# Kernel tuning notes

Measured on AMD Instinct MI355X. Metric: run time of the kernel, lower is better.

Reference implementation:

```python
import jax, jax.numpy as jnp
import numpy as np

N, E = 25000, 400000
NF, EF, HNF, HEF = 32, 32, 128, 128
NOUT, EOUT = 32, 32
D_N, D_E = HNF + NF, HEF + EF  # concat dims fed to the GNN layer


def _glorot(key, shape):
    return jax.random.normal(key, shape, jnp.float32) / np.sqrt(shape[0])


def setup_inputs() -> dict:
    key = jax.random.key(0)
    ks = jax.random.split(key, 10)
    return {
        "nf": jax.random.normal(ks[0], (N, NF), jnp.float32),
        "ef": jax.random.normal(ks[1], (E, EF), jnp.float32),
        "src": jax.random.randint(ks[2], (E,), 0, N),
        "dst": jax.random.randint(ks[3], (E,), 0, N),
        # AttnMPNNLayer params: edge model, attention logit model, node model
        "W_edge": _glorot(ks[4], (2 * D_N + D_E, HEF)),
        "b_edge": jnp.zeros((HEF,), jnp.float32),
        "W_attn": _glorot(ks[5], (2 * D_N + D_E, 1)),
        "b_attn": jnp.zeros((1,), jnp.float32),
        "W_node": _glorot(ks[6], (D_N + HEF, HNF)),
        "b_node": jnp.zeros((HNF,), jnp.float32),
        # output heads (MLP with num_neurons=[] -> single Linear)
        "W_nout": _glorot(ks[7], (HNF, NOUT)),
        "b_nout": jnp.zeros((NOUT,), jnp.float32),
        "W_eout": _glorot(ks[8], (HEF, EOUT)),
        "b_eout": jnp.zeros((EOUT,), jnp.float32),
        "n_iters": 3,
    }


def _attn_mpnn_layer(hnf, hef, src, dst, W_edge, b_edge, W_attn, b_attn, W_node, b_node):
    """Attention message passing: gather endpoints, edge MLP + attn logit,
    edge-softmax over incoming edges (per dst node), scatter-aggregate, node MLP."""
    n = hnf.shape[0]
    e_in = jnp.concatenate([hnf[src], hnf[dst], hef], axis=-1)   # [E, 2*D_N + D_E]
    m = jax.nn.relu(e_in @ W_edge + b_edge)                      # [E, HEF] new edge feats
    logit = (e_in @ W_attn + b_attn)[:, 0]                       # [E]
    # numerically stable edge softmax grouped by destination node
    lmax = jax.ops.segment_max(logit, dst, num_segments=n)
    lmax = jnp.where(jnp.isfinite(lmax), lmax, 0.0)              # isolated nodes -> 0
    a = jnp.exp(logit - lmax[dst])
    denom = jax.ops.segment_sum(a, dst, num_segments=n)
    alpha = a / jnp.maximum(denom[dst], 1e-16)
    agg = jax.ops.segment_sum(alpha[:, None] * m, dst, num_segments=n)  # [N, HEF]
    un = jax.nn.relu(jnp.concatenate([hnf, agg], axis=-1) @ W_node + b_node)  # [N, HNF]
    return un, m


def reference(nf, ef, src, dst, W_edge, b_edge, W_attn, b_attn, W_node, b_node,
              W_nout, b_nout, W_eout, b_eout, n_iters):
    hnf = jnp.zeros((nf.shape[0], HNF), nf.dtype)
    hef = jnp.zeros((ef.shape[0], HEF), ef.dtype)
    for _ in range(n_iters):
        hnf = jnp.concatenate([hnf, nf], axis=-1)   # input re-injection
        hef = jnp.concatenate([hef, ef], axis=-1)
        hnf, hef = _attn_mpnn_layer(hnf, hef, src, dst,
                                    W_edge, b_edge, W_attn, b_attn, W_node, b_node)
    unf = hnf @ W_nout + b_nout
    uef = hef @ W_eout + b_eout
    return unf, uef
```

## Files before the change

### kernel.cpp

```cpp
#include <hip/hip_runtime.h>


#define GN 25000
#define GE 400000
#define NODE_BLKS 196
#define EDGE_BLKS 3125

typedef unsigned short u16;
typedef __attribute__((ext_vector_type(8))) short bf16x8;
typedef __attribute__((ext_vector_type(4))) float f32x4;

__device__ inline float b2f(u16 v) {
  union { unsigned int u; float f; } x; x.u = ((unsigned int)v) << 16; return x.f;
}
__device__ inline u16 f2b(float f) {
  union { float f; unsigned int u; } x; x.f = f;
  unsigned int u = x.u;
  u += 0x7fffu + ((u >> 16) & 1u);
  return (u16)(u >> 16);
}

__global__ void detect_dtype(const void* nf, int* flag) {
  if (blockIdx.x == 0 && threadIdx.x == 0) {
    const u16* p = (const u16*)nf;
    int cnt = 0;
    for (int i = 0; i < 512; i += 2) {
      int e = (p[i] >> 7) & 0xFF;
      if (e >= 0x70 && e <= 0x85) cnt++;
    }
    *flag = (cnt < 128) ? 1 : 0;
  }
}

__global__ void convert_kernel(const void* src, u16* dst, long n, const int* flag) {
  int f32 = *flag;
  long i = (long)blockIdx.x * blockDim.x + threadIdx.x;
  long stride = (long)gridDim.x * blockDim.x;
  for (; i < n; i += stride)
    dst[i] = f32 ? f2b(((const float*)src)[i]) : ((const u16*)src)[i];
}

__global__ void gather_ef(const void* ef, const int* eid, u16* efc, const int* flag) {
  int f32 = *flag;
  long idx = (long)blockIdx.x * blockDim.x + threadIdx.x;
  long stride = (long)gridDim.x * blockDim.x;
  long ntot = (long)GE * 32;
  for (; idx < ntot; idx += stride) {
    long j = idx >> 5;
    int c = (int)(idx & 31);
    long e = eid[j];
    efc[idx] = f32 ? f2b(((const float*)ef)[e * 32 + c]) : ((const u16*)ef)[e * 32 + c];
  }
}

__global__ void gather_meta(const int* src, const int* dst, const int* eid,
                            int* srcs, int* dsts, int n) {
  int j = blockIdx.x * blockDim.x + threadIdx.x;
  if (j < n) { int e = eid[j]; srcs[j] = src[e]; dsts[j] = dst[e]; }
}

__global__ void prep_weights(const u16* We, const u16* Wn, const u16* Won, const u16* Woe,
                             u16* WeT, u16* WnpT, u16* WnuT, u16* WoN, u16* WoE) {
  int tid = blockIdx.x * blockDim.x + threadIdx.x;
  int nt = gridDim.x * blockDim.x;
  for (int i = tid; i < 128 * 160; i += nt) { int n = i / 160, k = i % 160; WeT[i] = We[(320 + k) * 128 + n]; }
  for (int i = tid; i < 256 * 160; i += nt) {
    int c = i / 160, k = i % 160;
    WnpT[i] = (c < 128) ? We[k * 128 + c] : We[(160 + k) * 128 + (c - 128)];
  }
  for (int i = tid; i < 128 * 288; i += nt) { int c = i / 288, k = i % 288; WnuT[i] = Wn[k * 128 + c]; }
  for (int i = tid; i < 32 * 128; i += nt) {
    int c = i / 128, k = i % 128;
    WoN[i] = Won[k * 32 + c];
    WoE[i] = Woe[k * 32 + c];
  }
}

__global__ void hist_kernel(const int* dst, int* counts, int n) {
  for (int e = blockIdx.x * blockDim.x + threadIdx.x; e < n; e += gridDim.x * blockDim.x)
    atomicAdd(&counts[dst[e]], 1);
}

__global__ __launch_bounds__(256) void scan_kernel(int* cursor, int* rowptr, int n) {
  __shared__ int part[256];
  int t = threadIdx.x;
  int per = (n + 255) / 256;
  int lo = t * per;
  int hi = lo + per; if (hi > n) hi = n;
  if (lo > n) lo = n;
  int s = 0;
  for (int i = lo; i < hi; ++i) s += cursor[i];
  part[t] = s;
  __syncthreads();
  for (int off = 1; off < 256; off <<= 1) {
    int v = (t >= off) ? part[t - off] : 0;
    __syncthreads();
    part[t] += v;
    __syncthreads();
  }
  int run = (t > 0) ? part[t - 1] : 0;
  for (int i = lo; i < hi; ++i) {
    int c = cursor[i];
    cursor[i] = run;
    rowptr[i + 1] = run + c;
    run += c;
  }
  if (t == 0) rowptr[0] = 0;
}

__global__ void fill_kernel(const int* dst, int* cursor, int* eid, int n) {
  for (int e = blockIdx.x * blockDim.x + threadIdx.x; e < n; e += gridDim.x * blockDim.x) {
    int p = atomicAdd(&cursor[dst[e]], 1);
    eid[p] = e;
  }
}

__global__ __launch_bounds__(256)
void node_proj(const u16* HNF, const u16* nf, const u16* WnpT, const u16* W_attn,
               u16* Xs, u16* Xd, float* as_, float* ad_, int kc0, int nrows) {
  __shared__ union {
    struct { __align__(16) u16 A[128][40]; __align__(16) u16 B[128][40]; } st;
    u16 C[128][130];
  } sm;
  __shared__ float dotbuf[128][2];
  int sel = blockIdx.y, blk = blockIdx.x, tid = threadIdx.x;
  int lane = tid & 63, wv = tid >> 6, wr = wv & 1, wc = wv >> 1;
  const u16* BT = WnpT + sel * 128 * 160;
  u16* OUT = sel ? Xd : Xs;
  float* AOUT = sel ? ad_ : as_;
  const u16* wa = W_attn + sel * 160;
  f32x4 acc[4][4];
  f32x4 zf = {0.f, 0.f, 0.f, 0.f};
  for (int i = 0; i < 4; ++i) for (int j = 0; j < 4; ++j) acc[i][j] = zf;
  float dp = 0.f;
  int arow = tid >> 1, ahalf = (tid & 1) * 16;
  int r0 = blk * 128;
  for (int kc = kc0; kc < 5; ++kc) {
    {
      int r = r0 + arow;
      uint4 v0 = make_uint4(0, 0, 0, 0), v1 = make_uint4(0, 0, 0, 0);
      if (r < nrows) {
        const uint4* p = (kc < 4) ? (const uint4*)(HNF + (size_t)r * 128 + kc * 32 + ahalf)
                                  : (const uint4*)(nf + (size_t)r * 32 + ahalf);
        v0 = p[0]; v1 = p[1];
      }
      *(uint4*)&sm.st.A[arow][ahalf] = v0;
      *(uint4*)&sm.st.A[arow][ahalf + 8] = v1;
    }
    {
      const uint4* p = (const uint4*)(BT + arow * 160 + kc * 32 + ahalf);
      uint4 v0 = p[0], v1 = p[1];
      *(uint4*)&sm.st.B[arow][ahalf] = v0;
      *(uint4*)&sm.st.B[arow][ahalf + 8] = v1;
    }
    __syncthreads();
    {
      float s = 0.f;
      for (int j = 0; j < 16; ++j) s += b2f(sm.st.A[arow][ahalf + j]) * b2f(wa[kc * 32 + ahalf + j]);
      dp += s;
    }
    int q = lane >> 4, l16 = lane & 15;
    bf16x8 af[4], bfr[4];
    for (int i = 0; i < 4; ++i) af[i] = *(const bf16x8*)&sm.st.A[wr * 64 + i * 16 + l16][q * 8];
    for (int j = 0; j < 4; ++j) bfr[j] = *(const bf16x8*)&sm.st.B[wc * 64 + j * 16 + l16][q * 8];
    for (int i = 0; i < 4; ++i)
      for (int j = 0; j < 4; ++j)
        acc[i][j] = __builtin_amdgcn_mfma_f32_16x16x32_bf16(af[i], bfr[j], acc[i][j], 0, 0, 0);
    __syncthreads();
  }
  dotbuf[arow][tid & 1] = dp;
  {
    int q = lane >> 4, l16 = lane & 15;
    for (int i = 0; i < 4; ++i)
      for (int j = 0; j < 4; ++j) {
        int col = wc * 64 + j * 16 + l16;
        for (int rr = 0; rr < 4; ++rr) {
          int row = wr * 64 + i * 16 + q * 4 + rr;
          sm.C[row][col] = f2b(acc[i][j][rr]);
        }
      }
  }
  __syncthreads();
  if (tid < 128) {
    int r = r0 + tid;
    if (r < nrows) AOUT[r] = dotbuf[tid][0] + dotbuf[tid][1];
  }
  {
    int r = tid >> 1, h = (tid & 1) * 64;
    int rg = r0 + r;
    if (rg < nrows) {
      uint4* po = (uint4*)(OUT + (size_t)rg * 128 + h);
      for (int k = 0; k < 8; ++k) {
        unsigned int a0 = *(const unsigned int*)&sm.C[r][h + k * 8];
        unsigned int a1 = *(const unsigned int*)&sm.C[r][h + k * 8 + 2];
        unsigned int a2 = *(const unsigned int*)&sm.C[r][h + k * 8 + 4];
        unsigned int a3 = *(const unsigned int*)&sm.C[r][h + k * 8 + 6];
        po[k] = make_uint4(a0, a1, a2, a3);
      }
    }
  }
}

__global__ __launch_bounds__(256, 4)
void edge_fused(u16* HEF, const u16* ef, const u16* WeT, const u16* W_attn,
                const u16* b_edge, const u16* b_attn, const int* srcs, const int* dsts,
                const u16* Xs, const u16* Xd, const float* as_, const float* ad_,
                float* logit, int kc0) {
  __shared__ union {
    struct { __align__(16) u16 A[128][40]; __align__(16) u16 B[128][40]; } st;
    float C[128][65];
  } sm;
  __shared__ float dotbuf[128];
  int blk = blockIdx.x, tid = threadIdx.x;
  int lane = tid & 63, wv = tid >> 6, wr = wv & 1, wc = wv >> 1;
  int q = lane >> 4, l16 = lane & 15;
  f32x4 acc[4][4];
  f32x4 zf = {0.f, 0.f, 0.f, 0.f};
  for (int i = 0; i < 4; ++i) for (int j = 0; j < 4; ++j) acc[i][j] = zf;
  float dp[4] = {0.f, 0.f, 0.f, 0.f};
  int arow = tid >> 1, ahalf = (tid & 1) * 16;
  long e0 = (long)blk * 128;
  const u16* wa = W_attn + 320;
  for (int kc = kc0; kc < 5; ++kc) {
    {
      long e = e0 + arow;
      const uint4* p = (kc < 4) ? (const uint4*)(HEF + e * 128 + kc * 32 + ahalf)
                                : (const uint4*)(ef + e * 32 + ahalf);
      uint4 v0 = p[0], v1 = p[1];
      *(uint4*)&sm.st.A[arow][ahalf] = v0;
      *(uint4*)&sm.st.A[arow][ahalf + 8] = v1;
    }
    {
      const uint4* p = (const uint4*)(WeT + arow * 160 + kc * 32 + ahalf);
      uint4 v0 = p[0], v1 = p[1];
      *(uint4*)&sm.st.B[arow][ahalf] = v0;
      *(uint4*)&sm.st.B[arow][ahalf + 8] = v1;
    }
    __syncthreads();
    bf16x8 af[4], bfr[4];
    for (int i = 0; i < 4; ++i) af[i] = *(const bf16x8*)&sm.st.A[wr * 64 + i * 16 + l16][q * 8];
    for (int j = 0; j < 4; ++j) bfr[j] = *(const bf16x8*)&sm.st.B[wc * 64 + j * 16 + l16][q * 8];
    if (wc == 0) {
      bf16x8 wv8 = *(const bf16x8*)&wa[kc * 32 + q * 8];
      float wf[8];
      for (int j = 0; j < 8; ++j) wf[j] = b2f((u16)wv8[j]);
      for (int i = 0; i < 4; ++i)
        for (int j = 0; j < 8; ++j) dp[i] += b2f((u16)af[i][j]) * wf[j];
    }
    for (int i = 0; i < 4; ++i)
      for (int j = 0; j < 4; ++j)
        acc[i][j] = __builtin_amdgcn_mfma_f32_16x16x32_bf16(af[i], bfr[j], acc[i][j], 0, 0, 0);
    __syncthreads();
  }
  if (wc == 0) {
    for (int i = 0; i < 4; ++i) {
      dp[i] += __shfl_xor(dp[i], 16);
      dp[i] += __shfl_xor(dp[i], 32);
    }
    if (q == 0)
      for (int i = 0; i < 4; ++i) dotbuf[wr * 64 + i * 16 + l16] = dp[i];
  }
  int r = tid >> 1;
  int h2 = (tid & 1) * 32;
  long e = e0 + r;
  int s = srcs[e], d = dsts[e];
  for (int p = 0; p < 2; ++p) {
    uint4 gvs[4], gvd[4];
    {
      const uint4* ps = (const uint4*)(Xs + (size_t)s * 128 + p * 64 + h2);
      const uint4* pd = (const uint4*)(Xd + (size_t)d * 128 + p * 64 + h2);
      for (int k = 0; k < 4; ++k) { gvs[k] = ps[k]; gvd[k] = pd[k]; }
    }
    if (wc == p) {
      for (int i = 0; i < 4; ++i)
        for (int j = 0; j < 4; ++j) {
          int col = j * 16 + l16;
          float bb = b2f(b_edge[p * 64 + col]);
          for (int rr = 0; rr < 4; ++rr) {
            int row = wr * 64 + i * 16 + q * 4 + rr;
            sm.C[row][col] = acc[i][j][rr] + bb;
          }
        }
    }
    __syncthreads();
    if (p == 0 && tid < 128) {
      long ee = e0 + tid;
      logit[ee] = dotbuf[tid] + as_[srcs[ee]] + ad_[dsts[ee]] + b2f(b_attn[0]);
    }
    uint4 o[4];
    for (int k = 0; k < 4; ++k) {
      unsigned int ov[4];
      for (int w = 0; w < 4; ++w) {
        int c = h2 + k * 8 + 2 * w;
        float c0 = sm.C[r][c], c1 = sm.C[r][c + 1];
        unsigned int us = ((const unsigned int*)&gvs[k])[w];
        unsigned int ud = ((const unsigned int*)&gvd[k])[w];
        float v0 = c0 + b2f((u16)(us & 0xffffu)) + b2f((u16)(ud & 0xffffu));
        float v1 = c1 + b2f((u16)(us >> 16)) + b2f((u16)(ud >> 16));
        v0 = fmaxf(v0, 0.f);
        v1 = fmaxf(v1, 0.f);
        ov[w] = (unsigned int)f2b(v0) | ((unsigned int)f2b(v1) << 16);
      }
      o[k] = make_uint4(ov[0], ov[1], ov[2], ov[3]);
    }
    {
      uint4* po = (uint4*)(HEF + e * 128 + p * 64 + h2);
      for (int k = 0; k < 4; ++k) po[k] = o[k];
    }
    if (p == 0) __syncthreads();
  }
}

__global__ __launch_bounds__(256)
void aggregate(const int* rowptr, const float* logit, const u16* M, u16* AGG, int nrows) {
  int gw = (blockIdx.x * blockDim.x + threadIdx.x) >> 6;
  int lane = threadIdx.x & 63;
  if (gw >= nrows) return;
  int beg = rowptr[gw], end = rowptr[gw + 1];
  float acc0 = 0.f, acc1 = 0.f;
  if (beg < end) {
    float mx = -1e30f;
    for (int j = beg + lane; j < end; j += 64) mx = fmaxf(mx, logit[j]);
    for (int off = 32; off > 0; off >>= 1) mx = fmaxf(mx, __shfl_xor(mx, off));
    float denom = 0.f;
    for (int j = beg; j < end; ++j) {
      float w = __expf(logit[j] - mx);
      denom += w;
      unsigned int mm = *(const unsigned int*)(M + (size_t)j * 128 + 2 * lane);
      acc0 += w * b2f((u16)(mm & 0xffffu));
      acc1 += w * b2f((u16)(mm >> 16));
    }
    float inv = 1.0f / fmaxf(denom, 1e-16f);
    acc0 *= inv; acc1 *= inv;
  }
  unsigned int out = (unsigned int)f2b(acc0) | ((unsigned int)f2b(acc1) << 16);
  *(unsigned int*)(AGG + (size_t)gw * 128 + 2 * lane) = out;
}

__global__ __launch_bounds__(256)
void node_update(u16* HNF, const u16* nf, const u16* AGG, const u16* WnuT,
                 const u16* b_node, int kc0, int nrows) {
  __shared__ union {
    struct { __align__(16) u16 A[128][40]; __align__(16) u16 B[128][40]; } st;
    u16 C[128][130];
  } sm;
  int blk = blockIdx.x, tid = threadIdx.x;
  int lane = tid & 63, wv = tid >> 6, wr = wv & 1, wc = wv >> 1;
  f32x4 acc[4][4];
  f32x4 zf = {0.f, 0.f, 0.f, 0.f};
  for (int i = 0; i < 4; ++i) for (int j = 0; j < 4; ++j) acc[i][j] = zf;
  int arow = tid >> 1, ahalf = (tid & 1) * 16;
  int r0 = blk * 128;
  for (int kc = kc0; kc < 9; ++kc) {
    {
      int r = r0 + arow;
      uint4 v0 = make_uint4(0, 0, 0, 0), v1 = make_uint4(0, 0, 0, 0);
      if (r < nrows) {
        const u16* p;
        if (kc < 4) p = HNF + (size_t)r * 128 + kc * 32 + ahalf;
        else if (kc == 4) p = nf + (size_t)r * 32 + ahalf;
        else p = AGG + (size_t)r * 128 + (kc - 5) * 32 + ahalf;
        v0 = ((const uint4*)p)[0];
        v1 = ((const uint4*)p)[1];
      }
      *(uint4*)&sm.st.A[arow][ahalf] = v0;
      *(uint4*)&sm.st.A[arow][ahalf + 8] = v1;
    }
    {
      const uint4* p = (const uint4*)(WnuT + arow * 288 + kc * 32 + ahalf);
      uint4 v0 = p[0], v1 = p[1];
      *(uint4*)&sm.st.B[arow][ahalf] = v0;
      *(uint4*)&sm.st.B[arow][ahalf + 8] = v1;
    }
    __syncthreads();
    int q = lane >> 4, l16 = lane & 15;
    bf16x8 af[4], bfr[4];
    for (int i = 0; i < 4; ++i) af[i] = *(const bf16x8*)&sm.st.A[wr * 64 + i * 16 + l16][q * 8];
    for (int j = 0; j < 4; ++j) bfr[j] = *(const bf16x8*)&sm.st.B[wc * 64 + j * 16 + l16][q * 8];
    for (int i = 0; i < 4; ++i)
      for (int j = 0; j < 4; ++j)
        acc[i][j] = __builtin_amdgcn_mfma_f32_16x16x32_bf16(af[i], bfr[j], acc[i][j], 0, 0, 0);
    __syncthreads();
  }
  int q = lane >> 4, l16 = lane & 15;
  for (int i = 0; i < 4; ++i)
    for (int j = 0; j < 4; ++j) {
      int col = wc * 64 + j * 16 + l16;
      float bb = b2f(b_node[col]);
      for (int rr = 0; rr < 4; ++rr) {
        int row = wr * 64 + i * 16 + q * 4 + rr;
        sm.C[row][col] = f2b(fmaxf(acc[i][j][rr] + bb, 0.f));
      }
    }
  __syncthreads();
  {
    int r = tid >> 1, h = (tid & 1) * 64;
    int rg = r0 + r;
    if (rg < nrows) {
      uint4* po = (uint4*)(HNF + (size_t)rg * 128 + h);
      for (int k = 0; k < 8; ++k) {
        unsigned int a0 = *(const unsigned int*)&sm.C[r][h + k * 8];
        unsigned int a1 = *(const unsigned int*)&sm.C[r][h + k * 8 + 2];
        unsigned int a2 = *(const unsigned int*)&sm.C[r][h + k * 8 + 4];
        unsigned int a3 = *(const unsigned int*)&sm.C[r][h + k * 8 + 6];
        po[k] = make_uint4(a0, a1, a2, a3);
      }
    }
  }
}

__global__ __launch_bounds__(256)
void head_kernel(const u16* IN, const u16* WT, const u16* bias, float* OUT, long R,
                 const int* remap) {
  __shared__ __align__(16) u16 Asm[128][40];
  __shared__ __align__(16) u16 Bsm[32][40];
  int blk = blockIdx.x, tid = threadIdx.x;
  int lane = tid & 63, wv = tid >> 6;
  f32x4 acc[2][2];
  f32x4 zf = {0.f, 0.f, 0.f, 0.f};
  for (int i = 0; i < 2; ++i) for (int j = 0; j < 2; ++j) acc[i][j] = zf;
  int arow = tid >> 1, ahalf = (tid & 1) * 16;
  long r0 = (long)blk * 128;
  for (int kc = 0; kc < 4; ++kc) {
    {
      long r = r0 + arow;
      uint4 v0 = make_uint4(0, 0, 0, 0), v1 = make_uint4(0, 0, 0, 0);
      if (r < R) {
        const uint4* p = (const uint4*)(IN + r * 128 + kc * 32 + ahalf);
        v0 = p[0]; v1 = p[1];
      }
      *(uint4*)&Asm[arow][ahalf] = v0;
      *(uint4*)&Asm[arow][ahalf + 8] = v1;
    }
    if (tid < 64) {
      const uint4* p = (const uint4*)(WT + arow * 128 + kc * 32 + ahalf);
      uint4 v0 = p[0], v1 = p[1];
      *(uint4*)&Bsm[arow][ahalf] = v0;
      *(uint4*)&Bsm[arow][ahalf + 8] = v1;
    }
    __syncthreads();
    int q = lane >> 4, l16 = lane & 15;
    bf16x8 af[2], bfr[2];
    for (int i = 0; i < 2; ++i) af[i] = *(const bf16x8*)&Asm[wv * 32 + i * 16 + l16][q * 8];
    for (int j = 0; j < 2; ++j) bfr[j] = *(const bf16x8*)&Bsm[j * 16 + l16][q * 8];
    for (int i = 0; i < 2; ++i)
      for (int j = 0; j < 2; ++j)
        acc[i][j] = __builtin_amdgcn_mfma_f32_16x16x32_bf16(af[i], bfr[j], acc[i][j], 0, 0, 0);
    __syncthreads();
  }
  int q = lane >> 4, l16 = lane & 15;
  for (int i = 0; i < 2; ++i)
    for (int rr = 0; rr < 4; ++rr) {
      long r = r0 + wv * 32 + i * 16 + q * 4 + rr;
      if (r < R) {
        long ro = remap ? (long)remap[r] : r;
        for (int j = 0; j < 2; ++j) {
          int col = j * 16 + l16;
          OUT[ro * 32 + col] = acc[i][j][rr] + b2f(bias[col]);
        }
      }
    }
}

extern "C" void kernel_launch(void* const* d_in, const int* in_sizes, int n_in,
                              void* d_out, int out_size, void* d_ws, size_t ws_size,
                              hipStream_t stream) {
  const size_t REQUIRED = 160000000;
  if (ws_size < REQUIRED) return;

  const void* nf_r = d_in[0];
  const void* ef_r = d_in[1];
  const int* src = (const int*)d_in[2];
  const int* dst = (const int*)d_in[3];

  char* ws = (char*)d_ws;
  auto alloc = [&](size_t bytes) {
    char* p = ws;
    ws += (bytes + 255) & ~(size_t)255;
    return p;
  };
  u16* HEF = (u16*)alloc((size_t)GE * 128 * 2);
  u16* HNF = (u16*)alloc((size_t)GN * 128 * 2);
  u16* Xs = (u16*)alloc((size_t)GN * 128 * 2);
  u16* Xd = (u16*)alloc((size_t)GN * 128 * 2);
  float* as_ = (float*)alloc((size_t)GN * 4);
  float* ad_ = (float*)alloc((size_t)GN * 4);
  float* logit = (float*)alloc((size_t)GE * 4);
  int* rowptr = (int*)alloc((size_t)(GN + 1) * 4);
  int* cursor = (int*)alloc((size_t)GN * 4);
  int* eid = (int*)alloc((size_t)GE * 4);
  int* srcs = (int*)alloc((size_t)GE * 4);
  int* dsts = (int*)alloc((size_t)GE * 4);
  u16* WeT = (u16*)alloc(128 * 160 * 2);
  u16* WnpT = (u16*)alloc(256 * 160 * 2);
  u16* WnuT = (u16*)alloc(128 * 288 * 2);
  u16* WoN = (u16*)alloc(32 * 128 * 2);
  u16* WoE = (u16*)alloc(32 * 128 * 2);
  u16* nfc = (u16*)alloc((size_t)GN * 32 * 2);
  u16* efc = (u16*)alloc((size_t)GE * 32 * 2);
  u16* Wec = (u16*)alloc(480 * 128 * 2);
  u16* bec = (u16*)alloc(128 * 2);
  u16* Wac = (u16*)alloc(480 * 2);
  u16* bac = (u16*)alloc(2);
  u16* Wnc = (u16*)alloc(288 * 128 * 2);
  u16* bnc = (u16*)alloc(128 * 2);
  u16* Wnoc = (u16*)alloc(128 * 32 * 2);
  u16* bnoc = (u16*)alloc(32 * 2);
  u16* Weoc = (u16*)alloc(128 * 32 * 2);
  u16* beoc = (u16*)alloc(32 * 2);
  int* dflag = (int*)alloc(4);
  u16* AGG = Xs;

  detect_dtype<<<1, 64, 0, stream>>>(nf_r, dflag);
  hipMemsetAsync(cursor, 0, (size_t)GN * 4, stream);
  hist_kernel<<<1563, 256, 0, stream>>>(dst, cursor, GE);
  scan_kernel<<<1, 256, 0, stream>>>(cursor, rowptr, GN);
  fill_kernel<<<1563, 256, 0, stream>>>(dst, cursor, eid, GE);

  convert_kernel<<<784, 256, 0, stream>>>(nf_r, nfc, (long)GN * 32, dflag);
  gather_ef<<<6250, 256, 0, stream>>>(ef_r, eid, efc, dflag);
  gather_meta<<<1563, 256, 0, stream>>>(src, dst, eid, srcs, dsts, GE);
  convert_kernel<<<240, 256, 0, stream>>>(d_in[4], Wec, 480 * 128, dflag);
  convert_kernel<<<1, 128, 0, stream>>>(d_in[5], bec, 128, dflag);
  convert_kernel<<<2, 256, 0, stream>>>(d_in[6], Wac, 480, dflag);
  convert_kernel<<<1, 64, 0, stream>>>(d_in[7], bac, 1, dflag);
  convert_kernel<<<144, 256, 0, stream>>>(d_in[8], Wnc, 288 * 128, dflag);
  convert_kernel<<<1, 128, 0, stream>>>(d_in[9], bnc, 128, dflag);
  convert_kernel<<<16, 256, 0, stream>>>(d_in[10], Wnoc, 128 * 32, dflag);
  convert_kernel<<<1, 64, 0, stream>>>(d_in[11], bnoc, 32, dflag);
  convert_kernel<<<16, 256, 0, stream>>>(d_in[12], Weoc, 128 * 32, dflag);
  convert_kernel<<<1, 64, 0, stream>>>(d_in[13], beoc, 32, dflag);
  prep_weights<<<128, 256, 0, stream>>>(Wec, Wnc, Wnoc, Weoc, WeT, WnpT, WnuT, WoN, WoE);

  for (int iter = 0; iter < 3; ++iter) {
    int kc0 = (iter == 0) ? 4 : 0;
    dim3 npgrid(NODE_BLKS, 2);
    node_proj<<<npgrid, 256, 0, stream>>>(HNF, nfc, WnpT, Wac, Xs, Xd, as_, ad_, kc0, GN);
    edge_fused<<<EDGE_BLKS, 256, 0, stream>>>(HEF, efc, WeT, Wac, bec, bac, srcs, dsts,
                                              Xs, Xd, as_, ad_, logit, kc0);
    aggregate<<<(GN + 3) / 4, 256, 0, stream>>>(rowptr, logit, HEF, AGG, GN);
    node_update<<<NODE_BLKS, 256, 0, stream>>>(HNF, nfc, AGG, WnuT, bnc, kc0, GN);
  }

  float* out_nf = (float*)d_out;
  float* out_ef = (float*)d_out + (size_t)GN * 32;
  head_kernel<<<NODE_BLKS, 256, 0, stream>>>(HNF, WoN, bnoc, out_nf, GN, nullptr);
  head_kernel<<<EDGE_BLKS, 256, 0, stream>>>(HEF, WoE, beoc, out_ef, GE, eid);
}
```

Before: 700.9 us.

## Shrink edge tiles, prefetch operands, vectorize aggregate, fuse setup kernels

```diff
diff --git a/kernel.cpp b/kernel.cpp
--- a/kernel.cpp
+++ b/kernel.cpp
@@ -4,7 +4,8 @@
 #define GN 25000
 #define GE 400000
 #define NODE_BLKS 196
-#define EDGE_BLKS 3125
+#define EDGE_BLKS 6250
+#define HEAD_EBLKS 3125
 
 typedef unsigned short u16;
 typedef __attribute__((ext_vector_type(8))) short bf16x8;
@@ -53,27 +54,34 @@
   }
 }
 
-__global__ void gather_meta(const int* src, const int* dst, const int* eid,
-                            int* srcs, int* dsts, int n) {
-  int j = blockIdx.x * blockDim.x + threadIdx.x;
-  if (j < n) { int e = eid[j]; srcs[j] = src[e]; dsts[j] = dst[e]; }
-}
-
-__global__ void prep_weights(const u16* We, const u16* Wn, const u16* Won, const u16* Woe,
-                             u16* WeT, u16* WnpT, u16* WnuT, u16* WoN, u16* WoE) {
+__global__ void prep_weights(const void* We, const void* Wn, const void* Wa,
+                             const void* Won, const void* Woe,
+                             const void* be, const void* ba, const void* bn,
+                             const void* bno, const void* beo,
+                             u16* WeT, u16* WnpT, u16* WnuT, u16* WoN, u16* WoE,
+                             u16* Wac, u16* bec, u16* bac, u16* bnc, u16* bnoc, u16* beoc,
+                             const int* flag) {
+  int f32 = *flag;
+  auto ld = [&](const void* p, long i) -> u16 {
+    return f32 ? f2b(((const float*)p)[i]) : ((const u16*)p)[i];
+  };
   int tid = blockIdx.x * blockDim.x + threadIdx.x;
   int nt = gridDim.x * blockDim.x;
-  for (int i = tid; i < 128 * 160; i += nt) { int n = i / 160, k = i % 160; WeT[i] = We[(320 + k) * 128 + n]; }
+  for (int i = tid; i < 128 * 160; i += nt) { int n = i / 160, k = i % 160; WeT[i] = ld(We, (long)(320 + k) * 128 + n); }
   for (int i = tid; i < 256 * 160; i += nt) {
     int c = i / 160, k = i % 160;
-    WnpT[i] = (c < 128) ? We[k * 128 + c] : We[(160 + k) * 128 + (c - 128)];
-  }
-  for (int i = tid; i < 128 * 288; i += nt) { int c = i / 288, k = i % 288; WnuT[i] = Wn[k * 128 + c]; }
+    WnpT[i] = (c < 128) ? ld(We, (long)k * 128 + c) : ld(We, (long)(160 + k) * 128 + (c - 128));
+  }
+  for (int i = tid; i < 128 * 288; i += nt) { int c = i / 288, k = i % 288; WnuT[i] = ld(Wn, (long)k * 128 + c); }
   for (int i = tid; i < 32 * 128; i += nt) {
     int c = i / 128, k = i % 128;
-    WoN[i] = Won[k * 32 + c];
-    WoE[i] = Woe[k * 32 + c];
-  }
+    WoN[i] = ld(Won, (long)k * 32 + c);
+    WoE[i] = ld(Woe, (long)k * 32 + c);
+  }
+  for (int i = tid; i < 480; i += nt) Wac[i] = ld(Wa, i);
+  for (int i = tid; i < 128; i += nt) { bec[i] = ld(be, i); bnc[i] = ld(bn, i); }
+  for (int i = tid; i < 32; i += nt) { bnoc[i] = ld(bno, i); beoc[i] = ld(beo, i); }
+  if (tid == 0) bac[0] = ld(ba, 0);
 }
 
 __global__ void hist_kernel(const int* dst, int* counts, int n) {
@@ -108,10 +116,14 @@
   if (t == 0) rowptr[0] = 0;
 }
 
-__global__ void fill_kernel(const int* dst, int* cursor, int* eid, int n) {
+__global__ void fill_kernel(const int* src, const int* dst, int* cursor, int* eid,
+                            int* srcs, int* dsts, int n) {
   for (int e = blockIdx.x * blockDim.x + threadIdx.x; e < n; e += gridDim.x * blockDim.x) {
-    int p = atomicAdd(&cursor[dst[e]], 1);
+    int d = dst[e];
+    int p = atomicAdd(&cursor[d], 1);
     eid[p] = e;
+    srcs[p] = src[e];
+    dsts[p] = d;
   }
 }
 
@@ -207,107 +219,103 @@
                 const u16* Xs, const u16* Xd, const float* as_, const float* ad_,
                 float* logit, int kc0) {
   __shared__ union {
-    struct { __align__(16) u16 A[128][40]; __align__(16) u16 B[128][40]; } st;
-    float C[128][65];
+    struct { __align__(16) u16 A[64][40]; __align__(16) u16 B[128][40]; } st;
+    float C[64][65];
   } sm;
-  __shared__ float dotbuf[128];
+  __shared__ float dotbuf[64];
   int blk = blockIdx.x, tid = threadIdx.x;
   int lane = tid & 63, wv = tid >> 6, wr = wv & 1, wc = wv >> 1;
   int q = lane >> 4, l16 = lane & 15;
-  f32x4 acc[4][4];
+  f32x4 acc[2][4];
   f32x4 zf = {0.f, 0.f, 0.f, 0.f};
-  for (int i = 0; i < 4; ++i) for (int j = 0; j < 4; ++j) acc[i][j] = zf;
-  float dp[4] = {0.f, 0.f, 0.f, 0.f};
-  int arow = tid >> 1, ahalf = (tid & 1) * 16;
-  long e0 = (long)blk * 128;
+  for (int i = 0; i < 2; ++i) for (int j = 0; j < 4; ++j) acc[i][j] = zf;
+  float dp[2] = {0.f, 0.f};
+  long e0 = (long)blk * 64;
+  long ea = e0 + (tid >> 2);
+  int qp = (tid & 3) * 8;
+  int brow = tid >> 1, bh = (tid & 1) * 16;
   const u16* wa = W_attn + 320;
+  uint4 va, vb0, vb1;
+  {
+    const uint4* pa = (kc0 < 4) ? (const uint4*)(HEF + ea * 128 + kc0 * 32 + qp)
+                                : (const uint4*)(ef + ea * 32 + qp);
+    va = pa[0];
+    const uint4* pb = (const uint4*)(WeT + brow * 160 + kc0 * 32 + bh);
+    vb0 = pb[0]; vb1 = pb[1];
+  }
   for (int kc = kc0; kc < 5; ++kc) {
-    {
-      long e = e0 + arow;
-      const uint4* p = (kc < 4) ? (const uint4*)(HEF + e * 128 + kc * 32 + ahalf)
-                                : (const uint4*)(ef + e * 32 + ahalf);
-      uint4 v0 = p[0], v1 = p[1];
-      *(uint4*)&sm.st.A[arow][ahalf] = v0;
-      *(uint4*)&sm.st.A[arow][ahalf + 8] = v1;
-    }
-    {
-      const uint4* p = (const uint4*)(WeT + arow * 160 + kc * 32 + ahalf);
-      uint4 v0 = p[0], v1 = p[1];
-      *(uint4*)&sm.st.B[arow][ahalf] = v0;
-      *(uint4*)&sm.st.B[arow][ahalf + 8] = v1;
-    }
-    __syncthreads();
-    bf16x8 af[4], bfr[4];
-    for (int i = 0; i < 4; ++i) af[i] = *(const bf16x8*)&sm.st.A[wr * 64 + i * 16 + l16][q * 8];
+    *(uint4*)&sm.st.A[tid >> 2][qp] = va;
+    *(uint4*)&sm.st.B[brow][bh] = vb0;
+    *(uint4*)&sm.st.B[brow][bh + 8] = vb1;
+    __syncthreads();
+    if (kc < 4) {
+      int kn = kc + 1;
+      const uint4* pa = (kn < 4) ? (const uint4*)(HEF + ea * 128 + kn * 32 + qp)
+                                 : (const uint4*)(ef + ea * 32 + qp);
+      va = pa[0];
+      const uint4* pb = (const uint4*)(WeT + brow * 160 + kn * 32 + bh);
+      vb0 = pb[0]; vb1 = pb[1];
+    }
+    bf16x8 af[2], bfr[4];
+    for (int i = 0; i < 2; ++i) af[i] = *(const bf16x8*)&sm.st.A[wr * 32 + i * 16 + l16][q * 8];
     for (int j = 0; j < 4; ++j) bfr[j] = *(const bf16x8*)&sm.st.B[wc * 64 + j * 16 + l16][q * 8];
     if (wc == 0) {
       bf16x8 wv8 = *(const bf16x8*)&wa[kc * 32 + q * 8];
       float wf[8];
       for (int j = 0; j < 8; ++j) wf[j] = b2f((u16)wv8[j]);
-      for (int i = 0; i < 4; ++i)
+      for (int i = 0; i < 2; ++i)
         for (int j = 0; j < 8; ++j) dp[i] += b2f((u16)af[i][j]) * wf[j];
     }
-    for (int i = 0; i < 4; ++i)
+    for (int i = 0; i < 2; ++i)
       for (int j = 0; j < 4; ++j)
         acc[i][j] = __builtin_amdgcn_mfma_f32_16x16x32_bf16(af[i], bfr[j], acc[i][j], 0, 0, 0);
     __syncthreads();
   }
   if (wc == 0) {
-    for (int i = 0; i < 4; ++i) {
+    for (int i = 0; i < 2; ++i) {
       dp[i] += __shfl_xor(dp[i], 16);
       dp[i] += __shfl_xor(dp[i], 32);
     }
     if (q == 0)
-      for (int i = 0; i < 4; ++i) dotbuf[wr * 64 + i * 16 + l16] = dp[i];
-  }
-  int r = tid >> 1;
-  int h2 = (tid & 1) * 32;
+      for (int i = 0; i < 2; ++i) dotbuf[wr * 32 + i * 16 + l16] = dp[i];
+  }
+  int r = tid >> 2, qh = tid & 3;
   long e = e0 + r;
   int s = srcs[e], d = dsts[e];
   for (int p = 0; p < 2; ++p) {
-    uint4 gvs[4], gvd[4];
-    {
-      const uint4* ps = (const uint4*)(Xs + (size_t)s * 128 + p * 64 + h2);
-      const uint4* pd = (const uint4*)(Xd + (size_t)d * 128 + p * 64 + h2);
-      for (int k = 0; k < 4; ++k) { gvs[k] = ps[k]; gvd[k] = pd[k]; }
-    }
+    int cb = p * 64 + qh * 16;
+    const uint4* ps = (const uint4*)(Xs + (size_t)s * 128 + cb);
+    const uint4* pd = (const uint4*)(Xd + (size_t)d * 128 + cb);
+    uint4 gs0 = ps[0], gs1 = ps[1], gd0 = pd[0], gd1 = pd[1];
+    if (p) __syncthreads();
     if (wc == p) {
-      for (int i = 0; i < 4; ++i)
+      for (int i = 0; i < 2; ++i)
         for (int j = 0; j < 4; ++j) {
           int col = j * 16 + l16;
           float bb = b2f(b_edge[p * 64 + col]);
-          for (int rr = 0; rr < 4; ++rr) {
-            int row = wr * 64 + i * 16 + q * 4 + rr;
-            sm.C[row][col] = acc[i][j][rr] + bb;
-          }
+          for (int rr = 0; rr < 4; ++rr)
+            sm.C[wr * 32 + i * 16 + q * 4 + rr][col] = acc[i][j][rr] + bb;
         }
     }
     __syncthreads();
-    if (p == 0 && tid < 128) {
+    if (p == 0 && tid < 64) {
       long ee = e0 + tid;
       logit[ee] = dotbuf[tid] + as_[srcs[ee]] + ad_[dsts[ee]] + b2f(b_attn[0]);
     }
-    uint4 o[4];
-    for (int k = 0; k < 4; ++k) {
-      unsigned int ov[4];
-      for (int w = 0; w < 4; ++w) {
-        int c = h2 + k * 8 + 2 * w;
-        float c0 = sm.C[r][c], c1 = sm.C[r][c + 1];
-        unsigned int us = ((const unsigned int*)&gvs[k])[w];
-        unsigned int ud = ((const unsigned int*)&gvd[k])[w];
-        float v0 = c0 + b2f((u16)(us & 0xffffu)) + b2f((u16)(ud & 0xffffu));
-        float v1 = c1 + b2f((u16)(us >> 16)) + b2f((u16)(ud >> 16));
-        v0 = fmaxf(v0, 0.f);
-        v1 = fmaxf(v1, 0.f);
-        ov[w] = (unsigned int)f2b(v0) | ((unsigned int)f2b(v1) << 16);
-      }
-      o[k] = make_uint4(ov[0], ov[1], ov[2], ov[3]);
-    }
-    {
-      uint4* po = (uint4*)(HEF + e * 128 + p * 64 + h2);
-      for (int k = 0; k < 4; ++k) po[k] = o[k];
-    }
-    if (p == 0) __syncthreads();
+    unsigned int us[8], ud[8];
+    *(uint4*)&us[0] = gs0; *(uint4*)&us[4] = gs1;
+    *(uint4*)&ud[0] = gd0; *(uint4*)&ud[4] = gd1;
+    unsigned int ov[8];
+    for (int w = 0; w < 8; ++w) {
+      float c0 = sm.C[r][qh * 16 + 2 * w];
+      float c1 = sm.C[r][qh * 16 + 2 * w + 1];
+      float v0 = c0 + b2f((u16)(us[w] & 0xffffu)) + b2f((u16)(ud[w] & 0xffffu));
+      float v1 = c1 + b2f((u16)(us[w] >> 16)) + b2f((u16)(ud[w] >> 16));
+      ov[w] = (unsigned int)f2b(fmaxf(v0, 0.f)) | ((unsigned int)f2b(fmaxf(v1, 0.f)) << 16);
+    }
+    uint4* po = (uint4*)(HEF + e * 128 + cb);
+    po[0] = *(uint4*)&ov[0];
+    po[1] = *(uint4*)&ov[4];
   }
 }
 
@@ -317,24 +325,40 @@
   int lane = threadIdx.x & 63;
   if (gw >= nrows) return;
   int beg = rowptr[gw], end = rowptr[gw + 1];
-  float acc0 = 0.f, acc1 = 0.f;
-  if (beg < end) {
-    float mx = -1e30f;
-    for (int j = beg + lane; j < end; j += 64) mx = fmaxf(mx, logit[j]);
-    for (int off = 32; off > 0; off >>= 1) mx = fmaxf(mx, __shfl_xor(mx, off));
-    float denom = 0.f;
-    for (int j = beg; j < end; ++j) {
-      float w = __expf(logit[j] - mx);
-      denom += w;
-      unsigned int mm = *(const unsigned int*)(M + (size_t)j * 128 + 2 * lane);
-      acc0 += w * b2f((u16)(mm & 0xffffu));
-      acc1 += w * b2f((u16)(mm >> 16));
-    }
-    float inv = 1.0f / fmaxf(denom, 1e-16f);
-    acc0 *= inv; acc1 *= inv;
-  }
-  unsigned int out = (unsigned int)f2b(acc0) | ((unsigned int)f2b(acc1) << 16);
-  *(unsigned int*)(AGG + (size_t)gw * 128 + 2 * lane) = out;
+  int sub = lane >> 4, cl = lane & 15;
+  float mx = -1e30f;
+  for (int j = beg + lane; j < end; j += 64) mx = fmaxf(mx, logit[j]);
+  for (int off = 32; off > 0; off >>= 1) mx = fmaxf(mx, __shfl_xor(mx, off));
+  float acc[8] = {0.f, 0.f, 0.f, 0.f, 0.f, 0.f, 0.f, 0.f};
+  float denom = 0.f;
+  for (int j0 = beg; j0 < end; j0 += 4) {
+    int j = j0 + sub;
+    float w = 0.f;
+    uint4 mv = make_uint4(0, 0, 0, 0);
+    if (j < end) {
+      w = __expf(logit[j] - mx);
+      mv = *(const uint4*)(M + (size_t)j * 128 + cl * 8);
+    }
+    denom += w;
+    const unsigned int* mw = (const unsigned int*)&mv;
+    for (int t = 0; t < 4; ++t) {
+      acc[2 * t]     += w * b2f((u16)(mw[t] & 0xffffu));
+      acc[2 * t + 1] += w * b2f((u16)(mw[t] >> 16));
+    }
+  }
+  denom += __shfl_xor(denom, 16);
+  denom += __shfl_xor(denom, 32);
+  for (int t = 0; t < 8; ++t) {
+    acc[t] += __shfl_xor(acc[t], 16);
+    acc[t] += __shfl_xor(acc[t], 32);
+  }
+  float inv = 1.0f / fmaxf(denom, 1e-16f);
+  if (sub == 0) {
+    unsigned int ov[4];
+    for (int t = 0; t < 4; ++t)
+      ov[t] = (unsigned int)f2b(acc[2 * t] * inv) | ((unsigned int)f2b(acc[2 * t + 1] * inv) << 16);
+    *(uint4*)(AGG + (size_t)gw * 128 + cl * 8) = *(uint4*)ov;
+  }
 }
 
 __global__ __launch_bounds__(256)
@@ -498,15 +522,11 @@
   u16* WoE = (u16*)alloc(32 * 128 * 2);
   u16* nfc = (u16*)alloc((size_t)GN * 32 * 2);
   u16* efc = (u16*)alloc((size_t)GE * 32 * 2);
-  u16* Wec = (u16*)alloc(480 * 128 * 2);
   u16* bec = (u16*)alloc(128 * 2);
   u16* Wac = (u16*)alloc(480 * 2);
   u16* bac = (u16*)alloc(2);
-  u16* Wnc = (u16*)alloc(288 * 128 * 2);
   u16* bnc = (u16*)alloc(128 * 2);
-  u16* Wnoc = (u16*)alloc(128 * 32 * 2);
   u16* bnoc = (u16*)alloc(32 * 2);
-  u16* Weoc = (u16*)alloc(128 * 32 * 2);
   u16* beoc = (u16*)alloc(32 * 2);
   int* dflag = (int*)alloc(4);
   u16* AGG = Xs;
@@ -515,22 +535,14 @@
   hipMemsetAsync(cursor, 0, (size_t)GN * 4, stream);
   hist_kernel<<<1563, 256, 0, stream>>>(dst, cursor, GE);
   scan_kernel<<<1, 256, 0, stream>>>(cursor, rowptr, GN);
-  fill_kernel<<<1563, 256, 0, stream>>>(dst, cursor, eid, GE);
+  fill_kernel<<<1563, 256, 0, stream>>>(src, dst, cursor, eid, srcs, dsts, GE);
 
   convert_kernel<<<784, 256, 0, stream>>>(nf_r, nfc, (long)GN * 32, dflag);
   gather_ef<<<6250, 256, 0, stream>>>(ef_r, eid, efc, dflag);
-  gather_meta<<<1563, 256, 0, stream>>>(src, dst, eid, srcs, dsts, GE);
-  convert_kernel<<<240, 256, 0, stream>>>(d_in[4], Wec, 480 * 128, dflag);
-  convert_kernel<<<1, 128, 0, stream>>>(d_in[5], bec, 128, dflag);
-  convert_kernel<<<2, 256, 0, stream>>>(d_in[6], Wac, 480, dflag);
-  convert_kernel<<<1, 64, 0, stream>>>(d_in[7], bac, 1, dflag);
-  convert_kernel<<<144, 256, 0, stream>>>(d_in[8], Wnc, 288 * 128, dflag);
-  convert_kernel<<<1, 128, 0, stream>>>(d_in[9], bnc, 128, dflag);
-  convert_kernel<<<16, 256, 0, stream>>>(d_in[10], Wnoc, 128 * 32, dflag);
-  convert_kernel<<<1, 64, 0, stream>>>(d_in[11], bnoc, 32, dflag);
-  convert_kernel<<<16, 256, 0, stream>>>(d_in[12], Weoc, 128 * 32, dflag);
-  convert_kernel<<<1, 64, 0, stream>>>(d_in[13], beoc, 32, dflag);
-  prep_weights<<<128, 256, 0, stream>>>(Wec, Wnc, Wnoc, Weoc, WeT, WnpT, WnuT, WoN, WoE);
+  prep_weights<<<128, 256, 0, stream>>>(d_in[4], d_in[8], d_in[6], d_in[10], d_in[12],
+                                        d_in[5], d_in[7], d_in[9], d_in[11], d_in[13],
+                                        WeT, WnpT, WnuT, WoN, WoE,
+                                        Wac, bec, bac, bnc, bnoc, beoc, dflag);
 
   for (int iter = 0; iter < 3; ++iter) {
     int kc0 = (iter == 0) ? 4 : 0;
@@ -545,5 +557,5 @@
   float* out_nf = (float*)d_out;
   float* out_ef = (float*)d_out + (size_t)GN * 32;
   head_kernel<<<NODE_BLKS, 256, 0, stream>>>(HNF, WoN, bnoc, out_nf, GN, nullptr);
-  head_kernel<<<EDGE_BLKS, 256, 0, stream>>>(HEF, WoE, beoc, out_ef, GE, eid);
-}
+  head_kernel<<<HEAD_EBLKS, 256, 0, stream>>>(HEF, WoE, beoc, out_ef, GE, eid);
+}
```

After: 641.7 us. 1.09x faster.
